# Optimization experiments

Hardware: AMD Instinct MI355X
Metric: run time of the kernel (lower is better)

The kernel has to match this reference:

```python
import jax, jax.numpy as jnp
import numpy as np

R, B, N, I, O, NB = 8, 4, 1024, 64, 64, 4
EPS = 1e-7  # keras.backend.epsilon()


def setup_inputs() -> dict:
    key = jax.random.key(0)
    ks = jax.random.split(key, 6)
    features = jax.random.normal(ks[0], (B, N, I), jnp.float32)
    adj = jax.random.randint(ks[1], (R, B, N, N), 0, 2, jnp.int32)  # stacked A[i]
    weight = jax.random.normal(ks[2], (NB, I, O), jnp.float32) * 0.1  # basis weights
    Wo = jax.random.normal(ks[3], (I, O), jnp.float32) * 0.1          # self-loop weight
    w_cmp = jax.random.normal(ks[4], (R, NB), jnp.float32) * 0.1      # basis coefficients
    b = jax.random.normal(ks[5], (O,), jnp.float32) * 0.1             # bias
    return {"features": features, "adj": adj, "weight": weight, "Wo": Wo, "w_cmp": w_cmp, "b": b}


def reference(features, adj, weight, Wo, w_cmp, b):
    # basis decomposition: per-relation weight [R, I, O]
    w_full = jnp.einsum('rb,bio->rio', w_cmp, weight)
    adj_f = adj.astype(features.dtype)                      # [R, B, N, N]
    # per-relation transform: x_r = features @ W_r -> [R, B, N, O]
    x = jnp.einsum('bni,rio->rbno', features, w_full)
    # batch_dot(edges^T, x): agg[r,b,n] = sum_m edges[r,b,m,n] * x[r,b,m]
    agg = jnp.einsum('rbmn,rbmo->rbno', adj_f, x)
    # original normalizer: K.sum(edges, axis=2, keepdims=True) -> row sums over last axis
    deg = adj_f.sum(axis=-1, keepdims=True)                 # [R, B, N, 1]
    agg = agg / (deg + EPS)
    self_x = features @ Wo                                  # [B, N, O]
    # concatenate [x_0 | x_1 | ... | x_{R-1} | self] along features
    concat = jnp.concatenate(
        [agg.transpose(1, 2, 0, 3).reshape(B, N, R * O), self_x], axis=-1
    )                                                       # [B, N, (R+1)*O]
    # faithful to original: reshape (..., O, R+1) then sum last axis
    out = concat.reshape(-1, N, O, R + 1).sum(axis=-1)      # [B, N, O]
    out = out + b
    return jax.nn.relu(out)
```

## Files before the change

kernel.cpp:

```cpp
#include <hip/hip_runtime.h>
#include <hip/hip_bf16.h>


#define NN 1024
#define EPSK 1e-7f

typedef __bf16 bf16x8 __attribute__((ext_vector_type(8)));
typedef float f32x4 __attribute__((ext_vector_type(4)));

__device__ __forceinline__ unsigned short f2bf(float f) {
  union { float f; unsigned int u; } v; v.f = f;
  return (unsigned short)((v.u + 0x7FFFu + ((v.u >> 16) & 1u)) >> 16);
}

__global__ __launch_bounds__(256) void prep_kernel(
    const float* __restrict__ feat,
    const float* __restrict__ weight,
    const float* __restrict__ Wo,
    const float* __restrict__ wcmp,
    unsigned short* __restrict__ xT,
    float* __restrict__ aggX,
    float* __restrict__ deg)
{
  __shared__ __align__(16) unsigned short featL[128 * 72];
  __shared__ __align__(16) float wTf[64 * 65];
  __shared__ __align__(16) unsigned short wfold[16 * 72];

  const int bid = blockIdx.x;
  const int t = threadIdx.x;
  const bool isSelf = bid >= 256;
  int r, b, chunk;
  if (!isSelf) { r = bid >> 5; b = (bid >> 3) & 3; chunk = bid & 7; }
  else { const int s2 = bid - 256; b = s2 >> 3; chunk = s2 & 7; r = 8; }
  const int n0 = chunk << 7;

  if (bid < 32) {
    for (int k = t; k < NN; k += 256) deg[bid * NN + k] = 0.0f;
  }

  const float* fsrc = feat + ((size_t)(b * NN + n0)) * 64;
  #pragma unroll
  for (int p = 0; p < 8; ++p) {
    const int idx = p * 256 + t;
    const int row = idx >> 4, c4 = idx & 15;
    const float4 v = *reinterpret_cast<const float4*>(fsrc + row * 64 + c4 * 4);
    ushort4 u;
    u.x = f2bf(v.x); u.y = f2bf(v.y); u.z = f2bf(v.z); u.w = f2bf(v.w);
    *reinterpret_cast<ushort4*>(&featL[row * 72 + c4 * 4]) = u;
  }

  if (!isSelf) {
    const float wc0 = wcmp[r * 4 + 0], wc1 = wcmp[r * 4 + 1];
    const float wc2 = wcmp[r * 4 + 2], wc3 = wcmp[r * 4 + 3];
    #pragma unroll
    for (int jj = 0; jj < 16; ++jj) {
      const int e = jj * 256 + t;
      const int i = e >> 6, c = e & 63;
      wTf[c * 65 + i] = wc0 * weight[i * 64 + c] + wc1 * weight[4096 + i * 64 + c] +
                        wc2 * weight[8192 + i * 64 + c] + wc3 * weight[12288 + i * 64 + c];
    }
  } else {
    #pragma unroll
    for (int jj = 0; jj < 16; ++jj) {
      const int e = jj * 256 + t;
      const int i = e >> 6, c = e & 63;
      wTf[c * 65 + i] = Wo[i * 64 + c];
    }
  }
  __syncthreads();

  #pragma unroll
  for (int jj = 0; jj < 4; ++jj) {
    const int e = jj * 256 + t;
    const int s = e >> 6, i = e & 63;
    float sum = 0.f;
    if (s < 8) {
      const int c0 = 9 * s - r;
      const int clo = c0 < 0 ? 0 : c0;
      const int chi = (c0 + 8 > 63) ? 63 : c0 + 8;
      for (int c = clo; c <= chi; ++c) sum += wTf[c * 65 + i];
    }
    wfold[s * 72 + i] = f2bf(sum);
  }
  __syncthreads();

  const int w = t >> 6, lane = t & 63;
  const int li = lane & 15, lg = lane >> 4;
  f32x4 acc0 = {0.f, 0.f, 0.f, 0.f}, acc1 = {0.f, 0.f, 0.f, 0.f};
  #pragma unroll
  for (int ks = 0; ks < 2; ++ks) {
    const int kof = ks * 32 + lg * 8;
    const bf16x8 af = __builtin_bit_cast(bf16x8,
        *reinterpret_cast<const uint4*>(&wfold[li * 72 + kof]));
    const bf16x8 b0 = __builtin_bit_cast(bf16x8,
        *reinterpret_cast<const uint4*>(&featL[((2 * w + 0) * 16 + li) * 72 + kof]));
    const bf16x8 b1 = __builtin_bit_cast(bf16x8,
        *reinterpret_cast<const uint4*>(&featL[((2 * w + 1) * 16 + li) * 72 + kof]));
    acc0 = __builtin_amdgcn_mfma_f32_16x16x32_bf16(af, b0, acc0, 0, 0, 0);
    acc1 = __builtin_amdgcn_mfma_f32_16x16x32_bf16(af, b1, acc1, 0, 0, 0);
  }
  if (!isSelf) {
    unsigned short* dst = xT + ((size_t)(r * 4 + b)) * (16 * NN);
    #pragma unroll
    for (int qq = 0; qq < 4; ++qq) {
      const int s = lg * 4 + qq;
      dst[s * NN + n0 + (2 * w + 0) * 16 + li] = f2bf(acc0[qq]);
      dst[s * NN + n0 + (2 * w + 1) * 16 + li] = f2bf(acc1[qq]);
    }
  } else {
    #pragma unroll
    for (int qq = 0; qq < 4; ++qq) {
      const int s = lg * 4 + qq;
      if (s < 8) {
        aggX[((size_t)(b * NN + n0 + (2 * w + 0) * 16 + li)) * 72 + 64 + s] = acc0[qq];
        aggX[((size_t)(b * NN + n0 + (2 * w + 1) * 16 + li)) * 72 + 64 + s] = acc1[qq];
      }
    }
  }
}

__global__ __launch_bounds__(256) void agg_kernel(
    const int* __restrict__ adj,
    const unsigned short* __restrict__ xT,
    float* __restrict__ aggX,
    float* __restrict__ deg)
{
  __shared__ __align__(16) unsigned short xlds[16 * 1032];
  __shared__ __align__(16) unsigned short adjT[2][64 * 40];
  __shared__ __align__(16) float degP[2][32][20];

  const int bid = blockIdx.x;
  const int rb = bid >> 4, r = rb >> 2, b = rb & 3;
  const int ncol0 = (bid & 15) << 6;
  const int t = threadIdx.x;
  const int q = t & 15, mp = t >> 4;

  const int* asrc = adj + (((size_t)rb) << 20) + ncol0 + (q << 2);

  int4 pA[4], pB[4];
  #pragma unroll
  for (int u = 0; u < 4; ++u) {
    pA[u] = *reinterpret_cast<const int4*>(asrc + ((size_t)(u * 32 + 2 * mp) << 10));
    pB[u] = *reinterpret_cast<const int4*>(asrc + ((size_t)(u * 32 + 2 * mp + 1) << 10));
  }

  const unsigned short* xs = xT + (((size_t)rb) << 14);
  #pragma unroll
  for (int it = 0; it < 8; ++it) {
    const int idx = t + (it << 8);
    const int row = idx >> 7, seg = idx & 127;
    *reinterpret_cast<uint4*>(&xlds[row * 1032 + seg * 8]) =
        *reinterpret_cast<const uint4*>(xs + row * NN + seg * 8);
  }

  const int w = t >> 6, lane = t & 63;
  const int li = lane & 15, lg = lane >> 4;
  const int arow = w * 16 + li;
  const int aoffs = arow * 40 + ((lg * 8) ^ ((w & 3) << 3));
  const int boffs = li * 1032 + lg * 8;

  f32x4 acc = {0.f, 0.f, 0.f, 0.f};

  for (int tt = 0; tt < 8; ++tt) {
    #pragma unroll
    for (int u = 0; u < 4; ++u) {
      const int s = tt * 4 + u;
      const int a0[4] = {pA[u].x, pA[u].y, pA[u].z, pA[u].w};
      const int a1[4] = {pB[u].x, pB[u].y, pB[u].z, pB[u].w};
      #pragma unroll
      for (int j = 0; j < 4; ++j) {
        const int row = (q << 2) + j;
        const int col = (mp << 1) ^ (((row >> 4) & 3) << 3);
        const unsigned int packed = (a0[j] ? 0x3F80u : 0u) | (a1[j] ? 0x3F800000u : 0u);
        *reinterpret_cast<unsigned int*>(&adjT[u & 1][row * 40 + col]) = packed;
      }
      degP[u & 1][2 * mp][q]     = (float)(a0[0] + a0[1] + a0[2] + a0[3]);
      degP[u & 1][2 * mp + 1][q] = (float)(a1[0] + a1[1] + a1[2] + a1[3]);

      if (s < 28) {
        const int* nsrc = asrc + ((size_t)((s + 4) * 32) << 10);
        pA[u] = *reinterpret_cast<const int4*>(nsrc + ((size_t)(2 * mp) << 10));
        pB[u] = *reinterpret_cast<const int4*>(nsrc + ((size_t)(2 * mp + 1) << 10));
      }

      asm volatile("s_waitcnt lgkmcnt(0)" ::: "memory");
      __builtin_amdgcn_s_barrier();

      if (t < 32) {
        float sum = 0.f;
        #pragma unroll
        for (int k4 = 0; k4 < 4; ++k4) {
          const float4 vv = *reinterpret_cast<const float4*>(&degP[u & 1][t][k4 * 4]);
          sum += vv.x + vv.y + vv.z + vv.w;
        }
        atomicAdd(&deg[rb * NN + s * 32 + t], sum);
      }

      const bf16x8 af = __builtin_bit_cast(bf16x8,
          *reinterpret_cast<const uint4*>(&adjT[u & 1][aoffs]));
      const bf16x8 bv = __builtin_bit_cast(bf16x8,
          *reinterpret_cast<const uint4*>(&xlds[boffs + s * 32]));
      acc = __builtin_amdgcn_mfma_f32_16x16x32_bf16(af, bv, acc, 0, 0, 0);
    }
  }

  float* dst = aggX + ((size_t)(b * NN + ncol0)) * 72 + r * 8;
  if (li < 8) {
    #pragma unroll
    for (int qq = 0; qq < 4; ++qq) {
      const int n = w * 16 + lg * 4 + qq;
      dst[(size_t)n * 72 + li] = acc[qq];
    }
  }
}

__global__ __launch_bounds__(256) void out_kernel(
    const float* __restrict__ aggX, const float* __restrict__ deg,
    const float* __restrict__ bias, float* __restrict__ out)
{
  const int gid = blockIdx.x * 256 + threadIdx.x;
  const int o = gid & 63;
  const int n = (gid >> 6) & 1023;
  const int b = gid >> 16;
  const float* cp = aggX + ((size_t)(b * NN + n)) * 72;

  const int r1 = (9 * o) >> 6;
  const int r2 = (9 * o + 8) >> 6;

  float v1 = cp[o + r1];
  if (r1 < 8) v1 /= (deg[(r1 * 4 + b) * NN + n] + EPSK);
  float acc = bias[o] + v1;
  if (r2 != r1) {
    float v2 = cp[o + r2];
    if (r2 < 8) v2 /= (deg[(r2 * 4 + b) * NN + n] + EPSK);
    acc += v2;
  }
  out[gid] = fmaxf(acc, 0.0f);
}

extern "C" void kernel_launch(void* const* d_in, const int* in_sizes, int n_in,
                              void* d_out, int out_size, void* d_ws, size_t ws_size,
                              hipStream_t stream) {
  const float* feat   = (const float*)d_in[0];
  const int*   adj    = (const int*)d_in[1];
  const float* weight = (const float*)d_in[2];
  const float* Wo     = (const float*)d_in[3];
  const float* wcmp   = (const float*)d_in[4];
  const float* bias   = (const float*)d_in[5];
  float* out = (float*)d_out;

  char* ws = (char*)d_ws;
  unsigned short* xT = (unsigned short*)(ws);
  float* aggX = (float*)(ws + 1048576u);
  float* deg  = (float*)(ws + 1048576u + 1179648u);

  prep_kernel<<<dim3(288), dim3(256), 0, stream>>>(feat, weight, Wo, wcmp, xT, aggX, deg);
  agg_kernel<<<dim3(512), dim3(256), 0, stream>>>(adj, xT, aggX, deg);
  out_kernel<<<dim3(1024), dim3(256), 0, stream>>>(aggX, deg, bias, out);
}
```

Before: 36.08 us.

## Deepen agg k-step to 64 rows, stage xT stores, fold self blocks into prep

The aggregation kernel now processes 64 adjacency rows per barrier step instead of 32. That halves the number of barriers and atomic degree updates, and it uses a byte-addressed XOR-swizzled LDS layout with two MFMAs per step. The prep kernel stages its bf16 outputs through LDS so xT is written with coalesced 16-byte stores. The separate self-loop blocks are folded into the r==0 blocks, shrinking the grid from 288 to 256. In exchange, each step holds more prefetch registers live, half the lanes load zeros for the B operand, and the r==0 prep blocks carry extra serial work.

```diff
diff --git a/kernel.cpp b/kernel.cpp
--- a/kernel.cpp
+++ b/kernel.cpp
@@ -25,13 +25,11 @@
   __shared__ __align__(16) unsigned short featL[128 * 72];
   __shared__ __align__(16) float wTf[64 * 65];
   __shared__ __align__(16) unsigned short wfold[16 * 72];
+  __shared__ __align__(16) unsigned short stg[16 * 136];
 
   const int bid = blockIdx.x;
   const int t = threadIdx.x;
-  const bool isSelf = bid >= 256;
-  int r, b, chunk;
-  if (!isSelf) { r = bid >> 5; b = (bid >> 3) & 3; chunk = bid & 7; }
-  else { const int s2 = bid - 256; b = s2 >> 3; chunk = s2 & 7; r = 8; }
+  const int r = bid >> 5, b = (bid >> 3) & 3, chunk = bid & 7;
   const int n0 = chunk << 7;
 
   if (bid < 32) {
@@ -49,7 +47,7 @@
     *reinterpret_cast<ushort4*>(&featL[row * 72 + c4 * 4]) = u;
   }
 
-  if (!isSelf) {
+  {
     const float wc0 = wcmp[r * 4 + 0], wc1 = wcmp[r * 4 + 1];
     const float wc2 = wcmp[r * 4 + 2], wc3 = wcmp[r * 4 + 3];
     #pragma unroll
@@ -58,13 +56,6 @@
       const int i = e >> 6, c = e & 63;
       wTf[c * 65 + i] = wc0 * weight[i * 64 + c] + wc1 * weight[4096 + i * 64 + c] +
                         wc2 * weight[8192 + i * 64 + c] + wc3 * weight[12288 + i * 64 + c];
-    }
-  } else {
-    #pragma unroll
-    for (int jj = 0; jj < 16; ++jj) {
-      const int e = jj * 256 + t;
-      const int i = e >> 6, c = e & 63;
-      wTf[c * 65 + i] = Wo[i * 64 + c];
     }
   }
   __syncthreads();
@@ -86,6 +77,7 @@
 
   const int w = t >> 6, lane = t & 63;
   const int li = lane & 15, lg = lane >> 4;
+
   f32x4 acc0 = {0.f, 0.f, 0.f, 0.f}, acc1 = {0.f, 0.f, 0.f, 0.f};
   #pragma unroll
   for (int ks = 0; ks < 2; ++ks) {
@@ -99,25 +91,117 @@
     acc0 = __builtin_amdgcn_mfma_f32_16x16x32_bf16(af, b0, acc0, 0, 0, 0);
     acc1 = __builtin_amdgcn_mfma_f32_16x16x32_bf16(af, b1, acc1, 0, 0, 0);
   }
-  if (!isSelf) {
-    unsigned short* dst = xT + ((size_t)(r * 4 + b)) * (16 * NN);
-    #pragma unroll
-    for (int qq = 0; qq < 4; ++qq) {
-      const int s = lg * 4 + qq;
-      dst[s * NN + n0 + (2 * w + 0) * 16 + li] = f2bf(acc0[qq]);
-      dst[s * NN + n0 + (2 * w + 1) * 16 + li] = f2bf(acc1[qq]);
-    }
-  } else {
+  #pragma unroll
+  for (int qq = 0; qq < 4; ++qq) {
+    const int s = lg * 4 + qq;
+    stg[s * 136 + (2 * w + 0) * 16 + li] = f2bf(acc0[qq]);
+    stg[s * 136 + (2 * w + 1) * 16 + li] = f2bf(acc1[qq]);
+  }
+  __syncthreads();
+  {
+    const int slot = t >> 4, seg = t & 15;
+    *reinterpret_cast<uint4*>(xT + ((size_t)(r * 4 + b) << 14) + slot * NN + n0 + seg * 8) =
+        *reinterpret_cast<const uint4*>(&stg[slot * 136 + seg * 8]);
+  }
+
+  if (r == 0) {
+    #pragma unroll
+    for (int jj = 0; jj < 16; ++jj) {
+      const int e = jj * 256 + t;
+      const int i = e >> 6, c = e & 63;
+      wTf[c * 65 + i] = Wo[i * 64 + c];
+    }
+    __syncthreads();
+    #pragma unroll
+    for (int jj = 0; jj < 4; ++jj) {
+      const int e = jj * 256 + t;
+      const int s = e >> 6, i = e & 63;
+      float sum = 0.f;
+      if (s < 8) {
+        const int c0 = 9 * s - 8;
+        const int clo = c0 < 0 ? 0 : c0;
+        const int chi = (c0 + 8 > 63) ? 63 : c0 + 8;
+        for (int c = clo; c <= chi; ++c) sum += wTf[c * 65 + i];
+      }
+      wfold[s * 72 + i] = f2bf(sum);
+    }
+    __syncthreads();
+    f32x4 sa0 = {0.f, 0.f, 0.f, 0.f}, sa1 = {0.f, 0.f, 0.f, 0.f};
+    #pragma unroll
+    for (int ks = 0; ks < 2; ++ks) {
+      const int kof = ks * 32 + lg * 8;
+      const bf16x8 af = __builtin_bit_cast(bf16x8,
+          *reinterpret_cast<const uint4*>(&wfold[li * 72 + kof]));
+      const bf16x8 b0 = __builtin_bit_cast(bf16x8,
+          *reinterpret_cast<const uint4*>(&featL[((2 * w + 0) * 16 + li) * 72 + kof]));
+      const bf16x8 b1 = __builtin_bit_cast(bf16x8,
+          *reinterpret_cast<const uint4*>(&featL[((2 * w + 1) * 16 + li) * 72 + kof]));
+      sa0 = __builtin_amdgcn_mfma_f32_16x16x32_bf16(af, b0, sa0, 0, 0, 0);
+      sa1 = __builtin_amdgcn_mfma_f32_16x16x32_bf16(af, b1, sa1, 0, 0, 0);
+    }
     #pragma unroll
     for (int qq = 0; qq < 4; ++qq) {
       const int s = lg * 4 + qq;
       if (s < 8) {
-        aggX[((size_t)(b * NN + n0 + (2 * w + 0) * 16 + li)) * 72 + 64 + s] = acc0[qq];
-        aggX[((size_t)(b * NN + n0 + (2 * w + 1) * 16 + li)) * 72 + 64 + s] = acc1[qq];
+        aggX[((size_t)(b * NN + n0 + (2 * w + 0) * 16 + li)) * 72 + 64 + s] = sa0[qq];
+        aggX[((size_t)(b * NN + n0 + (2 * w + 1) * 16 + li)) * 72 + 64 + s] = sa1[qq];
       }
     }
   }
 }
+
+#define AGG_STEP(P0, P1, P2, P3, S)                                               \
+  {                                                                               \
+    const int s_ = (S);                                                           \
+    const int buf_ = s_ & 1;                                                      \
+    unsigned char* at_ = &adjTB[buf_][0];                                         \
+    const int r0_[4] = {P0.x, P0.y, P0.z, P0.w};                                  \
+    const int r1_[4] = {P1.x, P1.y, P1.z, P1.w};                                  \
+    const int r2_[4] = {P2.x, P2.y, P2.z, P2.w};                                  \
+    const int r3_[4] = {P3.x, P3.y, P3.z, P3.w};                                  \
+    _Pragma("unroll")                                                             \
+    for (int jj = 0; jj < 4; ++jj) {                                              \
+      const int n_ = 4 * q + jj;                                                  \
+      const int key_ = ((n_ & 7) ^ ((n_ >> 3) & 7)) & 7;                          \
+      uint2 v_;                                                                   \
+      v_.x = (r0_[jj] ? 0x3F80u : 0u) | (r1_[jj] ? 0x3F800000u : 0u);             \
+      v_.y = (r2_[jj] ? 0x3F80u : 0u) | (r3_[jj] ? 0x3F800000u : 0u);             \
+      *reinterpret_cast<uint2*>(at_ + n_ * 128 + ((mp * 8) ^ (key_ << 4))) = v_;  \
+    }                                                                             \
+    degP[buf_][4 * mp + 0][q] = (float)(r0_[0] + r0_[1] + r0_[2] + r0_[3]);       \
+    degP[buf_][4 * mp + 1][q] = (float)(r1_[0] + r1_[1] + r1_[2] + r1_[3]);       \
+    degP[buf_][4 * mp + 2][q] = (float)(r2_[0] + r2_[1] + r2_[2] + r2_[3]);       \
+    degP[buf_][4 * mp + 3][q] = (float)(r3_[0] + r3_[1] + r3_[2] + r3_[3]);       \
+    if (s_ < 14) {                                                                \
+      const int* ns_ = asrc + ((size_t)((s_ + 2) * 64 + 4 * mp) << 10);           \
+      P0 = *reinterpret_cast<const int4*>(ns_);                                   \
+      P1 = *reinterpret_cast<const int4*>(ns_ + 1024);                            \
+      P2 = *reinterpret_cast<const int4*>(ns_ + 2048);                            \
+      P3 = *reinterpret_cast<const int4*>(ns_ + 3072);                            \
+    }                                                                             \
+    asm volatile("s_waitcnt lgkmcnt(0)" ::: "memory");                            \
+    __builtin_amdgcn_s_barrier();                                                 \
+    {                                                                             \
+      const int row_ = w * 16 + (lane >> 2), k4_ = lane & 3;                      \
+      const float4 f_ =                                                           \
+          *reinterpret_cast<const float4*>(&degP[buf_][row_][k4_ * 4]);           \
+      float sum_ = f_.x + f_.y + f_.z + f_.w;                                     \
+      sum_ += __shfl_xor(sum_, 1, 64);                                            \
+      sum_ += __shfl_xor(sum_, 2, 64);                                            \
+      if (k4_ == 0) atomicAdd(&deg[rb * NN + s_ * 64 + row_], sum_);              \
+    }                                                                             \
+    _Pragma("unroll")                                                             \
+    for (int h_ = 0; h_ < 2; ++h_) {                                              \
+      const bf16x8 af_ = __builtin_bit_cast(bf16x8,                               \
+          *reinterpret_cast<const uint4*>(                                        \
+              at_ + arow * 128 + ((h_ * 64 + lg * 16) ^ (keyA << 4))));           \
+      uint4 br_ = make_uint4(0u, 0u, 0u, 0u);                                     \
+      if (li < 8)                                                                 \
+        br_ = *reinterpret_cast<const uint4*>(&xlds[xbase + h_ * 32 + s_ * 64]);  \
+      acc = __builtin_amdgcn_mfma_f32_16x16x32_bf16(                              \
+          af_, __builtin_bit_cast(bf16x8, br_), acc, 0, 0, 0);                    \
+    }                                                                             \
+  }
 
 __global__ __launch_bounds__(256) void agg_kernel(
     const int* __restrict__ adj,
@@ -125,9 +209,9 @@
     float* __restrict__ aggX,
     float* __restrict__ deg)
 {
-  __shared__ __align__(16) unsigned short xlds[16 * 1032];
-  __shared__ __align__(16) unsigned short adjT[2][64 * 40];
-  __shared__ __align__(16) float degP[2][32][20];
+  __shared__ __align__(16) unsigned short xlds[16 * 1040];
+  __shared__ __align__(16) unsigned char adjTB[2][64 * 128];
+  __shared__ __align__(16) float degP[2][64][20];
 
   const int bid = blockIdx.x;
   const int rb = bid >> 4, r = rb >> 2, b = rb & 3;
@@ -137,71 +221,35 @@
 
   const int* asrc = adj + (((size_t)rb) << 20) + ncol0 + (q << 2);
 
-  int4 pA[4], pB[4];
-  #pragma unroll
-  for (int u = 0; u < 4; ++u) {
-    pA[u] = *reinterpret_cast<const int4*>(asrc + ((size_t)(u * 32 + 2 * mp) << 10));
-    pB[u] = *reinterpret_cast<const int4*>(asrc + ((size_t)(u * 32 + 2 * mp + 1) << 10));
-  }
+  int4 pa0 = *reinterpret_cast<const int4*>(asrc + ((size_t)(4 * mp + 0) << 10));
+  int4 pa1 = *reinterpret_cast<const int4*>(asrc + ((size_t)(4 * mp + 1) << 10));
+  int4 pa2 = *reinterpret_cast<const int4*>(asrc + ((size_t)(4 * mp + 2) << 10));
+  int4 pa3 = *reinterpret_cast<const int4*>(asrc + ((size_t)(4 * mp + 3) << 10));
+  int4 pb0 = *reinterpret_cast<const int4*>(asrc + ((size_t)(64 + 4 * mp + 0) << 10));
+  int4 pb1 = *reinterpret_cast<const int4*>(asrc + ((size_t)(64 + 4 * mp + 1) << 10));
+  int4 pb2 = *reinterpret_cast<const int4*>(asrc + ((size_t)(64 + 4 * mp + 2) << 10));
+  int4 pb3 = *reinterpret_cast<const int4*>(asrc + ((size_t)(64 + 4 * mp + 3) << 10));
 
   const unsigned short* xs = xT + (((size_t)rb) << 14);
   #pragma unroll
   for (int it = 0; it < 8; ++it) {
     const int idx = t + (it << 8);
     const int row = idx >> 7, seg = idx & 127;
-    *reinterpret_cast<uint4*>(&xlds[row * 1032 + seg * 8]) =
+    *reinterpret_cast<uint4*>(&xlds[row * 1040 + seg * 8]) =
         *reinterpret_cast<const uint4*>(xs + row * NN + seg * 8);
   }
 
   const int w = t >> 6, lane = t & 63;
   const int li = lane & 15, lg = lane >> 4;
   const int arow = w * 16 + li;
-  const int aoffs = arow * 40 + ((lg * 8) ^ ((w & 3) << 3));
-  const int boffs = li * 1032 + lg * 8;
+  const int keyA = ((arow & 7) ^ ((arow >> 3) & 7)) & 7;
+  const int xbase = li * 1040 + lg * 8;
 
   f32x4 acc = {0.f, 0.f, 0.f, 0.f};
 
   for (int tt = 0; tt < 8; ++tt) {
-    #pragma unroll
-    for (int u = 0; u < 4; ++u) {
-      const int s = tt * 4 + u;
-      const int a0[4] = {pA[u].x, pA[u].y, pA[u].z, pA[u].w};
-      const int a1[4] = {pB[u].x, pB[u].y, pB[u].z, pB[u].w};
-      #pragma unroll
-      for (int j = 0; j < 4; ++j) {
-        const int row = (q << 2) + j;
-        const int col = (mp << 1) ^ (((row >> 4) & 3) << 3);
-        const unsigned int packed = (a0[j] ? 0x3F80u : 0u) | (a1[j] ? 0x3F800000u : 0u);
-        *reinterpret_cast<unsigned int*>(&adjT[u & 1][row * 40 + col]) = packed;
-      }
-      degP[u & 1][2 * mp][q]     = (float)(a0[0] + a0[1] + a0[2] + a0[3]);
-      degP[u & 1][2 * mp + 1][q] = (float)(a1[0] + a1[1] + a1[2] + a1[3]);
-
-      if (s < 28) {
-        const int* nsrc = asrc + ((size_t)((s + 4) * 32) << 10);
-        pA[u] = *reinterpret_cast<const int4*>(nsrc + ((size_t)(2 * mp) << 10));
-        pB[u] = *reinterpret_cast<const int4*>(nsrc + ((size_t)(2 * mp + 1) << 10));
-      }
-
-      asm volatile("s_waitcnt lgkmcnt(0)" ::: "memory");
-      __builtin_amdgcn_s_barrier();
-
-      if (t < 32) {
-        float sum = 0.f;
-        #pragma unroll
-        for (int k4 = 0; k4 < 4; ++k4) {
-          const float4 vv = *reinterpret_cast<const float4*>(&degP[u & 1][t][k4 * 4]);
-          sum += vv.x + vv.y + vv.z + vv.w;
-        }
-        atomicAdd(&deg[rb * NN + s * 32 + t], sum);
-      }
-
-      const bf16x8 af = __builtin_bit_cast(bf16x8,
-          *reinterpret_cast<const uint4*>(&adjT[u & 1][aoffs]));
-      const bf16x8 bv = __builtin_bit_cast(bf16x8,
-          *reinterpret_cast<const uint4*>(&xlds[boffs + s * 32]));
-      acc = __builtin_amdgcn_mfma_f32_16x16x32_bf16(af, bv, acc, 0, 0, 0);
-    }
+    AGG_STEP(pa0, pa1, pa2, pa3, 2 * tt);
+    AGG_STEP(pb0, pb1, pb2, pb3, 2 * tt + 1);
   }
 
   float* dst = aggX + ((size_t)(b * NN + ncol0)) * 72 + r * 8;
@@ -254,7 +302,7 @@
   float* aggX = (float*)(ws + 1048576u);
   float* deg  = (float*)(ws + 1048576u + 1179648u);
 
-  prep_kernel<<<dim3(288), dim3(256), 0, stream>>>(feat, weight, Wo, wcmp, xT, aggX, deg);
+  prep_kernel<<<dim3(256), dim3(256), 0, stream>>>(feat, weight, Wo, wcmp, xT, aggX, deg);
   agg_kernel<<<dim3(512), dim3(256), 0, stream>>>(adj, xT, aggX, deg);
   out_kernel<<<dim3(1024), dim3(256), 0, stream>>>(aggX, deg, bias, out);
 }
```

After: 37.16 us. +3.0%, slower.

## Coalesce xT stores via LDS, remap agg blocks, parallelize degree reduction

Applied to the files above, without the earlier changes.

In the prep kernel, the scattered 2-byte stores of xT are staged through a shared-memory tile and written back as 16-byte vectors, so global writes are coalesced. In the agg kernel, the block-to-(relation, batch, column) mapping is reordered to spread work across relations differently, and a barrier is added before the main loop. The per-step degree reduction now uses all 256 threads with wave shuffles instead of 32 threads each doing 16 adds, which shortens the serial tail after every barrier. The loop body becomes a macro with no change in logic, and the extra staging adds a barrier and some LDS in prep.

```diff
diff --git a/kernel.cpp b/kernel.cpp
--- a/kernel.cpp
+++ b/kernel.cpp
@@ -25,6 +25,7 @@
   __shared__ __align__(16) unsigned short featL[128 * 72];
   __shared__ __align__(16) float wTf[64 * 65];
   __shared__ __align__(16) unsigned short wfold[16 * 72];
+  __shared__ __align__(16) unsigned short stg[16 * 136];
 
   const int bid = blockIdx.x;
   const int t = threadIdx.x;
@@ -86,6 +87,7 @@
 
   const int w = t >> 6, lane = t & 63;
   const int li = lane & 15, lg = lane >> 4;
+
   f32x4 acc0 = {0.f, 0.f, 0.f, 0.f}, acc1 = {0.f, 0.f, 0.f, 0.f};
   #pragma unroll
   for (int ks = 0; ks < 2; ++ks) {
@@ -99,14 +101,18 @@
     acc0 = __builtin_amdgcn_mfma_f32_16x16x32_bf16(af, b0, acc0, 0, 0, 0);
     acc1 = __builtin_amdgcn_mfma_f32_16x16x32_bf16(af, b1, acc1, 0, 0, 0);
   }
+
   if (!isSelf) {
-    unsigned short* dst = xT + ((size_t)(r * 4 + b)) * (16 * NN);
     #pragma unroll
     for (int qq = 0; qq < 4; ++qq) {
       const int s = lg * 4 + qq;
-      dst[s * NN + n0 + (2 * w + 0) * 16 + li] = f2bf(acc0[qq]);
-      dst[s * NN + n0 + (2 * w + 1) * 16 + li] = f2bf(acc1[qq]);
-    }
+      stg[s * 136 + (2 * w + 0) * 16 + li] = f2bf(acc0[qq]);
+      stg[s * 136 + (2 * w + 1) * 16 + li] = f2bf(acc1[qq]);
+    }
+    __syncthreads();
+    const int slot = t >> 4, seg = t & 15;
+    *reinterpret_cast<uint4*>(xT + ((size_t)(r * 4 + b) << 14) + slot * NN + n0 + seg * 8) =
+        *reinterpret_cast<const uint4*>(&stg[slot * 136 + seg * 8]);
   } else {
     #pragma unroll
     for (int qq = 0; qq < 4; ++qq) {
@@ -118,6 +124,47 @@
     }
   }
 }
+
+#define AGG_STEP(U, S)                                                            \
+  {                                                                               \
+    const int s_ = (S);                                                           \
+    const int buf_ = s_ & 1;                                                      \
+    unsigned short* at_ = &adjT[buf_][0];                                         \
+    const int a0_[4] = {pA[U].x, pA[U].y, pA[U].z, pA[U].w};                      \
+    const int a1_[4] = {pB[U].x, pB[U].y, pB[U].z, pB[U].w};                      \
+    _Pragma("unroll")                                                             \
+    for (int jj = 0; jj < 4; ++jj) {                                              \
+      const int row_ = (q << 2) + jj;                                             \
+      const int col_ = (mp << 1) ^ (((row_ >> 4) & 3) << 3);                      \
+      const unsigned int packed_ =                                                \
+          (a0_[jj] ? 0x3F80u : 0u) | (a1_[jj] ? 0x3F800000u : 0u);                \
+      *reinterpret_cast<unsigned int*>(&at_[row_ * 40 + col_]) = packed_;         \
+    }                                                                             \
+    degP[buf_][2 * mp][q]     = (float)(a0_[0] + a0_[1] + a0_[2] + a0_[3]);       \
+    degP[buf_][2 * mp + 1][q] = (float)(a1_[0] + a1_[1] + a1_[2] + a1_[3]);       \
+    if (s_ < 28) {                                                                \
+      const int* ns_ = asrc + ((size_t)((s_ + 4) * 32) << 10);                    \
+      pA[U] = *reinterpret_cast<const int4*>(ns_ + ((size_t)(2 * mp) << 10));     \
+      pB[U] = *reinterpret_cast<const int4*>(ns_ + ((size_t)(2 * mp + 1) << 10)); \
+    }                                                                             \
+    asm volatile("s_waitcnt lgkmcnt(0)" ::: "memory");                            \
+    __builtin_amdgcn_s_barrier();                                                 \
+    {                                                                             \
+      const int row_ = t >> 3, j_ = t & 7;                                        \
+      const float2 d2_ =                                                          \
+          *reinterpret_cast<const float2*>(&degP[buf_][row_][2 * j_]);            \
+      float sum_ = d2_.x + d2_.y;                                                 \
+      sum_ += __shfl_xor(sum_, 1, 64);                                            \
+      sum_ += __shfl_xor(sum_, 2, 64);                                            \
+      sum_ += __shfl_xor(sum_, 4, 64);                                            \
+      if (j_ == 0) atomicAdd(&deg[rb * NN + s_ * 32 + row_], sum_);               \
+    }                                                                             \
+    const bf16x8 af_ = __builtin_bit_cast(bf16x8,                                 \
+        *reinterpret_cast<const uint4*>(&at_[aoffs]));                            \
+    const bf16x8 bv_ = __builtin_bit_cast(bf16x8,                                 \
+        *reinterpret_cast<const uint4*>(&xlds[boffs + s_ * 32]));                 \
+    acc = __builtin_amdgcn_mfma_f32_16x16x32_bf16(af_, bv_, acc, 0, 0, 0);        \
+  }
 
 __global__ __launch_bounds__(256) void agg_kernel(
     const int* __restrict__ adj,
@@ -130,8 +177,11 @@
   __shared__ __align__(16) float degP[2][32][20];
 
   const int bid = blockIdx.x;
-  const int rb = bid >> 4, r = rb >> 2, b = rb & 3;
-  const int ncol0 = (bid & 15) << 6;
+  const int qq2 = bid & 255, hi = bid >> 8;
+  const int r = ((qq2 & 3) << 1) | hi;
+  const int b = (qq2 >> 2) & 3;
+  const int rb = r * 4 + b;
+  const int ncol0 = (qq2 >> 4) << 6;
   const int t = threadIdx.x;
   const int q = t & 15, mp = t >> 4;
 
@@ -161,47 +211,13 @@
 
   f32x4 acc = {0.f, 0.f, 0.f, 0.f};
 
+  __syncthreads();
+
   for (int tt = 0; tt < 8; ++tt) {
-    #pragma unroll
-    for (int u = 0; u < 4; ++u) {
-      const int s = tt * 4 + u;
-      const int a0[4] = {pA[u].x, pA[u].y, pA[u].z, pA[u].w};
-      const int a1[4] = {pB[u].x, pB[u].y, pB[u].z, pB[u].w};
-      #pragma unroll
-      for (int j = 0; j < 4; ++j) {
-        const int row = (q << 2) + j;
-        const int col = (mp << 1) ^ (((row >> 4) & 3) << 3);
-        const unsigned int packed = (a0[j] ? 0x3F80u : 0u) | (a1[j] ? 0x3F800000u : 0u);
-        *reinterpret_cast<unsigned int*>(&adjT[u & 1][row * 40 + col]) = packed;
-      }
-      degP[u & 1][2 * mp][q]     = (float)(a0[0] + a0[1] + a0[2] + a0[3]);
-      degP[u & 1][2 * mp + 1][q] = (float)(a1[0] + a1[1] + a1[2] + a1[3]);
-
-      if (s < 28) {
-        const int* nsrc = asrc + ((size_t)((s + 4) * 32) << 10);
-        pA[u] = *reinterpret_cast<const int4*>(nsrc + ((size_t)(2 * mp) << 10));
-        pB[u] = *reinterpret_cast<const int4*>(nsrc + ((size_t)(2 * mp + 1) << 10));
-      }
-
-      asm volatile("s_waitcnt lgkmcnt(0)" ::: "memory");
-      __builtin_amdgcn_s_barrier();
-
-      if (t < 32) {
-        float sum = 0.f;
-        #pragma unroll
-        for (int k4 = 0; k4 < 4; ++k4) {
-          const float4 vv = *reinterpret_cast<const float4*>(&degP[u & 1][t][k4 * 4]);
-          sum += vv.x + vv.y + vv.z + vv.w;
-        }
-        atomicAdd(&deg[rb * NN + s * 32 + t], sum);
-      }
-
-      const bf16x8 af = __builtin_bit_cast(bf16x8,
-          *reinterpret_cast<const uint4*>(&adjT[u & 1][aoffs]));
-      const bf16x8 bv = __builtin_bit_cast(bf16x8,
-          *reinterpret_cast<const uint4*>(&xlds[boffs + s * 32]));
-      acc = __builtin_amdgcn_mfma_f32_16x16x32_bf16(af, bv, acc, 0, 0, 0);
-    }
+    AGG_STEP(0, 4 * tt + 0);
+    AGG_STEP(1, 4 * tt + 1);
+    AGG_STEP(2, 4 * tt + 2);
+    AGG_STEP(3, 4 * tt + 3);
   }
 
   float* dst = aggX + ((size_t)(b * NN + ncol0)) * 72 + r * 8;
```

New measurement: 37.40 us. 3.7% more time.

## Replace MFMA adjacency aggregation with FP32 FMA split-K tiles and partial sums

Applied to the files above, without the earlier changes.

The aggregation kernel drops the bf16 MFMA path, which transposed and packed adjacency into LDS with a barrier every step, in favour of scalar FP32 FMAs. Each block now handles a 256x256 tile of one relation/batch adjacency with a four-deep register prefetch, and writes split-K partial sums that the output kernel adds across four slabs. Node features are stored as fp32 [n,8] through LDS staging for coalesced writes. This removes the per-step barriers and bf16 conversion, but adds scalar FMA work, a larger partial-sum buffer, and extra reads in the output kernel.

```diff
diff --git a/kernel.cpp b/kernel.cpp
--- a/kernel.cpp
+++ b/kernel.cpp
@@ -18,13 +18,14 @@
     const float* __restrict__ weight,
     const float* __restrict__ Wo,
     const float* __restrict__ wcmp,
-    unsigned short* __restrict__ xT,
-    float* __restrict__ aggX,
+    float* __restrict__ xf,
+    float* __restrict__ selfP,
     float* __restrict__ deg)
 {
   __shared__ __align__(16) unsigned short featL[128 * 72];
   __shared__ __align__(16) float wTf[64 * 65];
   __shared__ __align__(16) unsigned short wfold[16 * 72];
+  __shared__ __align__(16) float stg[128 * 8];
 
   const int bid = blockIdx.x;
   const int t = threadIdx.x;
@@ -86,6 +87,7 @@
 
   const int w = t >> 6, lane = t & 63;
   const int li = lane & 15, lg = lane >> 4;
+
   f32x4 acc0 = {0.f, 0.f, 0.f, 0.f}, acc1 = {0.f, 0.f, 0.f, 0.f};
   #pragma unroll
   for (int ks = 0; ks < 2; ++ks) {
@@ -99,141 +101,162 @@
     acc0 = __builtin_amdgcn_mfma_f32_16x16x32_bf16(af, b0, acc0, 0, 0, 0);
     acc1 = __builtin_amdgcn_mfma_f32_16x16x32_bf16(af, b1, acc1, 0, 0, 0);
   }
-  if (!isSelf) {
-    unsigned short* dst = xT + ((size_t)(r * 4 + b)) * (16 * NN);
+
+  if (lg < 2) {
     #pragma unroll
     for (int qq = 0; qq < 4; ++qq) {
       const int s = lg * 4 + qq;
-      dst[s * NN + n0 + (2 * w + 0) * 16 + li] = f2bf(acc0[qq]);
-      dst[s * NN + n0 + (2 * w + 1) * 16 + li] = f2bf(acc1[qq]);
-    }
-  } else {
-    #pragma unroll
-    for (int qq = 0; qq < 4; ++qq) {
-      const int s = lg * 4 + qq;
-      if (s < 8) {
-        aggX[((size_t)(b * NN + n0 + (2 * w + 0) * 16 + li)) * 72 + 64 + s] = acc0[qq];
-        aggX[((size_t)(b * NN + n0 + (2 * w + 1) * 16 + li)) * 72 + 64 + s] = acc1[qq];
-      }
-    }
+      stg[((2 * w + 0) * 16 + li) * 8 + s] = acc0[qq];
+      stg[((2 * w + 1) * 16 + li) * 8 + s] = acc1[qq];
+    }
+  }
+  __syncthreads();
+  {
+    float* dstF = isSelf ? (selfP + ((size_t)(b * NN + n0)) * 8)
+                         : (xf + ((size_t)((r * 4 + b) * NN + n0)) * 8);
+    *reinterpret_cast<float4*>(dstF + t * 4) =
+        *reinterpret_cast<const float4*>(&stg[t * 4]);
   }
 }
 
 __global__ __launch_bounds__(256) void agg_kernel(
     const int* __restrict__ adj,
-    const unsigned short* __restrict__ xT,
-    float* __restrict__ aggX,
+    const float* __restrict__ xf,
+    float* __restrict__ aggP,
     float* __restrict__ deg)
 {
-  __shared__ __align__(16) unsigned short xlds[16 * 1032];
-  __shared__ __align__(16) unsigned short adjT[2][64 * 40];
-  __shared__ __align__(16) float degP[2][32][20];
+  __shared__ __align__(16) float xsL[256 * 8];
+  __shared__ __align__(16) float degL[256 * 66];
 
   const int bid = blockIdx.x;
-  const int rb = bid >> 4, r = rb >> 2, b = rb & 3;
-  const int ncol0 = (bid & 15) << 6;
+  const int rb = bid >> 4, mq = (bid >> 2) & 3, nq = bid & 3;
   const int t = threadIdx.x;
-  const int q = t & 15, mp = t >> 4;
-
-  const int* asrc = adj + (((size_t)rb) << 20) + ncol0 + (q << 2);
-
-  int4 pA[4], pB[4];
-  #pragma unroll
-  for (int u = 0; u < 4; ++u) {
-    pA[u] = *reinterpret_cast<const int4*>(asrc + ((size_t)(u * 32 + 2 * mp) << 10));
-    pB[u] = *reinterpret_cast<const int4*>(asrc + ((size_t)(u * 32 + 2 * mp + 1) << 10));
-  }
-
-  const unsigned short* xs = xT + (((size_t)rb) << 14);
-  #pragma unroll
-  for (int it = 0; it < 8; ++it) {
-    const int idx = t + (it << 8);
-    const int row = idx >> 7, seg = idx & 127;
-    *reinterpret_cast<uint4*>(&xlds[row * 1032 + seg * 8]) =
-        *reinterpret_cast<const uint4*>(xs + row * NN + seg * 8);
-  }
-
-  const int w = t >> 6, lane = t & 63;
-  const int li = lane & 15, lg = lane >> 4;
-  const int arow = w * 16 + li;
-  const int aoffs = arow * 40 + ((lg * 8) ^ ((w & 3) << 3));
-  const int boffs = li * 1032 + lg * 8;
-
-  f32x4 acc = {0.f, 0.f, 0.f, 0.f};
-
-  for (int tt = 0; tt < 8; ++tt) {
-    #pragma unroll
-    for (int u = 0; u < 4; ++u) {
-      const int s = tt * 4 + u;
-      const int a0[4] = {pA[u].x, pA[u].y, pA[u].z, pA[u].w};
-      const int a1[4] = {pB[u].x, pB[u].y, pB[u].z, pB[u].w};
-      #pragma unroll
-      for (int j = 0; j < 4; ++j) {
-        const int row = (q << 2) + j;
-        const int col = (mp << 1) ^ (((row >> 4) & 3) << 3);
-        const unsigned int packed = (a0[j] ? 0x3F80u : 0u) | (a1[j] ? 0x3F800000u : 0u);
-        *reinterpret_cast<unsigned int*>(&adjT[u & 1][row * 40 + col]) = packed;
-      }
-      degP[u & 1][2 * mp][q]     = (float)(a0[0] + a0[1] + a0[2] + a0[3]);
-      degP[u & 1][2 * mp + 1][q] = (float)(a1[0] + a1[1] + a1[2] + a1[3]);
-
-      if (s < 28) {
-        const int* nsrc = asrc + ((size_t)((s + 4) * 32) << 10);
-        pA[u] = *reinterpret_cast<const int4*>(nsrc + ((size_t)(2 * mp) << 10));
-        pB[u] = *reinterpret_cast<const int4*>(nsrc + ((size_t)(2 * mp + 1) << 10));
-      }
-
-      asm volatile("s_waitcnt lgkmcnt(0)" ::: "memory");
-      __builtin_amdgcn_s_barrier();
-
-      if (t < 32) {
-        float sum = 0.f;
-        #pragma unroll
-        for (int k4 = 0; k4 < 4; ++k4) {
-          const float4 vv = *reinterpret_cast<const float4*>(&degP[u & 1][t][k4 * 4]);
-          sum += vv.x + vv.y + vv.z + vv.w;
-        }
-        atomicAdd(&deg[rb * NN + s * 32 + t], sum);
-      }
-
-      const bf16x8 af = __builtin_bit_cast(bf16x8,
-          *reinterpret_cast<const uint4*>(&adjT[u & 1][aoffs]));
-      const bf16x8 bv = __builtin_bit_cast(bf16x8,
-          *reinterpret_cast<const uint4*>(&xlds[boffs + s * 32]));
-      acc = __builtin_amdgcn_mfma_f32_16x16x32_bf16(af, bv, acc, 0, 0, 0);
-    }
-  }
-
-  float* dst = aggX + ((size_t)(b * NN + ncol0)) * 72 + r * 8;
-  if (li < 8) {
-    #pragma unroll
-    for (int qq = 0; qq < 4; ++qq) {
-      const int n = w * 16 + lg * 4 + qq;
-      dst[(size_t)n * 72 + li] = acc[qq];
-    }
+  const int tm = t >> 6, tn = t & 63;
+  const int mbase = mq << 8, nbase = nq << 8;
+
+  {
+    const float* xs = xf + ((size_t)(rb * NN + mbase)) * 8;
+    *reinterpret_cast<float4*>(&xsL[t * 8]) = *reinterpret_cast<const float4*>(xs + t * 8);
+    *reinterpret_cast<float4*>(&xsL[t * 8 + 4]) = *reinterpret_cast<const float4*>(xs + t * 8 + 4);
+  }
+
+  const int* asrc = adj + (((size_t)rb) << 20) + ((size_t)mbase << 10) + nbase + (tn << 2);
+
+  float acc[4][8];
+  #pragma unroll
+  for (int j = 0; j < 4; ++j)
+    #pragma unroll
+    for (int s = 0; s < 8; ++s) acc[j][s] = 0.f;
+
+  __syncthreads();
+
+  int4 buf0 = *reinterpret_cast<const int4*>(asrc + ((size_t)(0 * 4 + tm) << 10));
+  int4 buf1 = *reinterpret_cast<const int4*>(asrc + ((size_t)(1 * 4 + tm) << 10));
+  int4 buf2 = *reinterpret_cast<const int4*>(asrc + ((size_t)(2 * 4 + tm) << 10));
+  int4 buf3 = *reinterpret_cast<const int4*>(asrc + ((size_t)(3 * 4 + tm) << 10));
+
+#define AGG_BODY(BUF, I)                                                        \
+  {                                                                             \
+    const int4 cur_ = BUF;                                                      \
+    const int ml_ = ((I) << 2) + tm;                                            \
+    if ((I) < 60) {                                                             \
+      BUF = *reinterpret_cast<const int4*>(asrc + ((size_t)(ml_ + 16) << 10));  \
+    }                                                                           \
+    const float a0_ = (float)cur_.x, a1_ = (float)cur_.y;                       \
+    const float a2_ = (float)cur_.z, a3_ = (float)cur_.w;                       \
+    degL[ml_ * 66 + tn] = (float)(cur_.x + cur_.y + cur_.z + cur_.w);           \
+    const float4 xlo_ = *reinterpret_cast<const float4*>(&xsL[ml_ * 8]);        \
+    const float4 xhi_ = *reinterpret_cast<const float4*>(&xsL[ml_ * 8 + 4]);    \
+    const float xs_[8] = {xlo_.x, xlo_.y, xlo_.z, xlo_.w,                       \
+                          xhi_.x, xhi_.y, xhi_.z, xhi_.w};                      \
+    _Pragma("unroll")                                                           \
+    for (int s_ = 0; s_ < 8; ++s_) {                                            \
+      acc[0][s_] = fmaf(a0_, xs_[s_], acc[0][s_]);                              \
+      acc[1][s_] = fmaf(a1_, xs_[s_], acc[1][s_]);                              \
+      acc[2][s_] = fmaf(a2_, xs_[s_], acc[2][s_]);                              \
+      acc[3][s_] = fmaf(a3_, xs_[s_], acc[3][s_]);                              \
+    }                                                                           \
+  }
+
+  for (int ib = 0; ib < 16; ++ib) {
+    AGG_BODY(buf0, ib * 4 + 0);
+    AGG_BODY(buf1, ib * 4 + 1);
+    AGG_BODY(buf2, ib * 4 + 2);
+    AGG_BODY(buf3, ib * 4 + 3);
+  }
+#undef AGG_BODY
+
+  __syncthreads();
+
+  {
+    float s = 0.f;
+    #pragma unroll
+    for (int k = 0; k < 32; ++k) {
+      const float2 v = *reinterpret_cast<const float2*>(&degL[t * 66 + 2 * k]);
+      s += v.x + v.y;
+    }
+    atomicAdd(&deg[rb * NN + mbase + t], s);
+  }
+  __syncthreads();
+
+  float* accL = degL;
+  #pragma unroll
+  for (int j = 0; j < 4; ++j) {
+    *reinterpret_cast<float4*>(&accL[t * 36 + j * 8]) =
+        make_float4(acc[j][0], acc[j][1], acc[j][2], acc[j][3]);
+    *reinterpret_cast<float4*>(&accL[t * 36 + j * 8 + 4]) =
+        make_float4(acc[j][4], acc[j][5], acc[j][6], acc[j][7]);
+  }
+  __syncthreads();
+  {
+    const int nl = t;
+    const int tn2 = nl >> 2, j2 = nl & 3;
+    float o8[8];
+    #pragma unroll
+    for (int s = 0; s < 8; ++s) o8[s] = 0.f;
+    #pragma unroll
+    for (int tm2 = 0; tm2 < 4; ++tm2) {
+      const int base = (tm2 * 64 + tn2) * 36 + j2 * 8;
+      const float4 lo = *reinterpret_cast<const float4*>(&accL[base]);
+      const float4 hi = *reinterpret_cast<const float4*>(&accL[base + 4]);
+      o8[0] += lo.x; o8[1] += lo.y; o8[2] += lo.z; o8[3] += lo.w;
+      o8[4] += hi.x; o8[5] += hi.y; o8[6] += hi.z; o8[7] += hi.w;
+    }
+    float* dst = aggP + (((size_t)(mq * 32 + rb)) * NN + nbase + nl) * 8;
+    *reinterpret_cast<float4*>(dst) = make_float4(o8[0], o8[1], o8[2], o8[3]);
+    *reinterpret_cast<float4*>(dst + 4) = make_float4(o8[4], o8[5], o8[6], o8[7]);
   }
 }
 
 __global__ __launch_bounds__(256) void out_kernel(
-    const float* __restrict__ aggX, const float* __restrict__ deg,
+    const float* __restrict__ aggP,
+    const float* __restrict__ selfP,
+    const float* __restrict__ deg,
     const float* __restrict__ bias, float* __restrict__ out)
 {
   const int gid = blockIdx.x * 256 + threadIdx.x;
   const int o = gid & 63;
   const int n = (gid >> 6) & 1023;
   const int b = gid >> 16;
-  const float* cp = aggX + ((size_t)(b * NN + n)) * 72;
 
   const int r1 = (9 * o) >> 6;
   const int r2 = (9 * o + 8) >> 6;
 
-  float v1 = cp[o + r1];
-  if (r1 < 8) v1 /= (deg[(r1 * 4 + b) * NN + n] + EPSK);
-  float acc = bias[o] + v1;
-  if (r2 != r1) {
-    float v2 = cp[o + r2];
-    if (r2 < 8) v2 /= (deg[(r2 * 4 + b) * NN + n] + EPSK);
-    acc += v2;
+  float acc = bias[o];
+  #pragma unroll
+  for (int pass = 0; pass < 2; ++pass) {
+    const int r = pass ? r2 : r1;
+    if (pass && r2 == r1) break;
+    const int s = o - 7 * r;
+    float v;
+    if (r < 8) {
+      const size_t base = (((size_t)(r * 4 + b)) * NN + n) * 8 + s;
+      v = aggP[base] + aggP[base + 262144] + aggP[base + 524288] + aggP[base + 786432];
+      v /= (deg[(r * 4 + b) * NN + n] + EPSK);
+    } else {
+      v = selfP[((size_t)(b * NN + n)) * 8 + (o - 56)];
+    }
+    acc += v;
   }
   out[gid] = fmaxf(acc, 0.0f);
 }
@@ -250,11 +273,12 @@
   float* out = (float*)d_out;
 
   char* ws = (char*)d_ws;
-  unsigned short* xT = (unsigned short*)(ws);
-  float* aggX = (float*)(ws + 1048576u);
-  float* deg  = (float*)(ws + 1048576u + 1179648u);
-
-  prep_kernel<<<dim3(288), dim3(256), 0, stream>>>(feat, weight, Wo, wcmp, xT, aggX, deg);
-  agg_kernel<<<dim3(512), dim3(256), 0, stream>>>(adj, xT, aggX, deg);
-  out_kernel<<<dim3(1024), dim3(256), 0, stream>>>(aggX, deg, bias, out);
-}
+  float* xf    = (float*)(ws);
+  float* selfP = (float*)(ws + 1048576u);
+  float* aggP  = (float*)(ws + 1048576u + 131072u);
+  float* deg   = (float*)(ws + 1048576u + 131072u + 4194304u);
+
+  prep_kernel<<<dim3(288), dim3(256), 0, stream>>>(feat, weight, Wo, wcmp, xf, selfP, deg);
+  agg_kernel<<<dim3(512), dim3(256), 0, stream>>>(adj, xf, aggP, deg);
+  out_kernel<<<dim3(1024), dim3(256), 0, stream>>>(aggP, selfP, deg, bias, out);
+}
```

Result: faster. 35.24 us (-2.3%).
